# Kernel tuning notes

Measured on AMD Instinct MI355X. Metric: run time of the kernel, lower is better.

The kernel has to match this reference:

```python
import jax, jax.numpy as jnp
import numpy as np

N_NODES = 50000


def _gcn_layer(x, src, dst, norm_src, norm_dst, W, b, act):
    # DGL GraphConv with norm='both': D_out^{-1/2} A D_in^{-1/2} X W + b
    h = x * norm_src[:, None]                      # scale by src out-degree
    m = h[src]                                     # gather messages [E, d]
    agg = jax.ops.segment_sum(m, dst, num_segments=N_NODES)  # scatter-add
    agg = agg * norm_dst[:, None]
    out = agg @ W + b
    if act:
        out = jax.nn.relu(out)
    return out


def setup_inputs() -> dict:
    key = jax.random.key(0)
    ks = jax.random.split(key, 10)
    E = 800000
    in_size, hid, out_size = 128, 128, 64
    features = jax.random.normal(ks[0], (N_NODES, in_size), dtype=jnp.float32)
    src = jax.random.randint(ks[1], (E,), 0, N_NODES, dtype=jnp.int32)
    dst = jax.random.randint(ks[2], (E,), 0, N_NODES, dtype=jnp.int32)
    s = 0.05
    W1 = jax.random.normal(ks[3], (in_size, hid), dtype=jnp.float32) * s
    b1 = jnp.zeros((hid,), dtype=jnp.float32)
    W2 = jax.random.normal(ks[4], (hid, hid), dtype=jnp.float32) * s
    b2 = jnp.zeros((hid,), dtype=jnp.float32)
    W3 = jax.random.normal(ks[5], (hid, out_size), dtype=jnp.float32) * s
    b3 = jnp.zeros((out_size,), dtype=jnp.float32)
    return {"features": features, "W1": W1, "b1": b1, "W2": W2, "b2": b2,
            "W3": W3, "b3": b3, "src": src, "dst": dst}


def reference(features, W1, b1, W2, b2, W3, b3, src, dst):
    ones = jnp.ones(src.shape, dtype=features.dtype)
    out_deg = jax.ops.segment_sum(ones, src, num_segments=N_NODES)
    in_deg = jax.ops.segment_sum(ones, dst, num_segments=N_NODES)
    norm_src = jnp.maximum(out_deg, 1.0) ** -0.5   # clamp(min=1) as in DGL
    norm_dst = jnp.maximum(in_deg, 1.0) ** -0.5
    h = _gcn_layer(features, src, dst, norm_src, norm_dst, W1, b1, act=True)
    # dropout is identity in eval mode
    h = _gcn_layer(h, src, dst, norm_src, norm_dst, W2, b2, act=True)
    h = _gcn_layer(h, src, dst, norm_src, norm_dst, W3, b3, act=False)
    return h
```

## Files before the change

kernel.cpp:

```cpp
#include <hip/hip_runtime.h>
#include <math.h>

#define N_NODES 50000
#define K_DIM 128
#define CAP 64
#define CHUNK 12500
#define RH 25000
#define HWORDS 12500

typedef __attribute__((ext_vector_type(8))) short short8_t;
typedef __attribute__((ext_vector_type(8))) unsigned short ushort8_t;
typedef __attribute__((ext_vector_type(4))) float f32x4_t;
typedef __attribute__((ext_vector_type(8))) _Float16 half8_t;

__device__ inline unsigned short f2bf(float x) {
    unsigned u = __float_as_uint(x);
    unsigned r = u + 0x7fffu + ((u >> 16) & 1u);
    return (unsigned short)(r >> 16);
}
__device__ inline float bf2f(unsigned short h) {
    return __uint_as_float(((unsigned)h) << 16);
}

__global__ __launch_bounds__(1024) void hist_init_split_kernel(
        const int* __restrict__ src, const int* __restrict__ dst, int E,
        unsigned* __restrict__ pin, unsigned* __restrict__ pout,
        _Float16* Yx, _Float16* Yy, _Float16* Yz,
        const float* __restrict__ W1, const float* __restrict__ W2,
        const float* __restrict__ W3,
        unsigned short* __restrict__ W1h, unsigned short* __restrict__ W1l,
        unsigned short* __restrict__ W2h, unsigned short* __restrict__ W2l,
        unsigned short* __restrict__ W3h, unsigned short* __restrict__ W3l,
        int NBLK) {
    int tid = threadIdx.x;
    if (blockIdx.x < (unsigned)(NBLK * 4)) {
        __shared__ unsigned h[HWORDS];
        int b  = blockIdx.x >> 2;
        int io = (blockIdx.x >> 1) & 1;
        int r  = blockIdx.x & 1;
        for (int t = tid; t < HWORDS; t += 1024) h[t] = 0;
        __syncthreads();
        const int* keys = io ? src : dst;
        int start = b * CHUNK;
        int end = start + CHUNK; if (end > E) end = E;
        int vlo = r * RH;
        for (int i = start + tid; i < end; i += 1024) {
            int v = keys[i] - vlo;
            if ((unsigned)v < (unsigned)RH)
                atomicAdd(&h[v >> 1], 1u << ((v & 1) * 16));
        }
        __syncthreads();
        unsigned* out = io ? pout : pin;
        for (int t = tid; t < HWORDS; t += 1024)
            out[(size_t)b * (2 * HWORDS) + r * HWORDS + t] = h[t];
        return;
    }
    if (blockIdx.x == (unsigned)(NBLK * 4)) {
        if (tid < 128) {
            Yx[(size_t)N_NODES * 128 + tid] = (_Float16)0.f;
            Yy[(size_t)N_NODES * 128 + tid] = (_Float16)0.f;
        }
        if (tid < 64) Yz[(size_t)N_NODES * 64 + tid] = (_Float16)0.f;
        return;
    }
    int gi = (blockIdx.x - (NBLK * 4 + 1)) * 1024 + tid;
    const float* W; unsigned short *WBh, *WBl; int M, i;
    if (gi < 2048)      { W = W1; WBh = W1h; WBl = W1l; M = 128; i = gi; }
    else if (gi < 4096) { W = W2; WBh = W2h; WBl = W2l; M = 128; i = gi - 2048; }
    else if (gi < 5120) { W = W3; WBh = W3h; WBl = W3l; M = 64;  i = gi - 4096; }
    else return;
    int c    = i >> 8;
    int rem  = i & 255;
    int kc   = rem >> 6;
    int lane = rem & 63;
    int m = lane & 15, q = lane >> 4;
    int n = c * 16 + m;
    #pragma unroll
    for (int j = 0; j < 8; ++j) {
        int k = kc * 32 + q * 8 + j;
        float w = W[(size_t)k * M + n];
        unsigned short hi = f2bf(w);
        unsigned short lo = f2bf(w - bf2f(hi));
        WBh[(size_t)i * 8 + j] = hi;
        WBl[(size_t)i * 8 + j] = lo;
    }
}

__global__ void offsets_norm_kernel(const unsigned* __restrict__ pin,
                                    const unsigned* __restrict__ pout,
                                    unsigned short* __restrict__ off16,
                                    int* __restrict__ indeg,
                                    float* __restrict__ nsrc, float* __restrict__ ndst,
                                    int n, int NB) {
    int v = blockIdx.x * blockDim.x + threadIdx.x;
    if (v >= n) return;
    int wi = v >> 1, sh = (v & 1) * 16;
    int od = 0;
    for (int b = 0; b < NB; ++b)
        od += (pout[(size_t)b * (2 * HWORDS) + wi] >> sh) & 0xffff;
    int run = 0;
    for (int b = 0; b < NB; ++b) {
        int c = (pin[(size_t)b * (2 * HWORDS) + wi] >> sh) & 0xffff;
        off16[(size_t)b * n + v] = (unsigned short)(run < CAP ? run : CAP);
        run += c;
    }
    indeg[v] = run < CAP ? run : CAP;
    int odc = od < 1 ? 1 : od;
    int idc = run < 1 ? 1 : run;
    nsrc[v] = 1.0f / sqrtf((float)odc);
    ndst[v] = 1.0f / sqrtf((float)idc);
}

__global__ __launch_bounds__(512) void scatter_gemm_kernel(
        const int* __restrict__ src, const int* __restrict__ dst, int E,
        const unsigned short* __restrict__ off16,
        unsigned short* __restrict__ csr, int n, int NB2,
        const float* __restrict__ X,
        const unsigned short* __restrict__ WBh_,
        const unsigned short* __restrict__ WBl_,
        const float* __restrict__ nsrc, _Float16* __restrict__ Yh) {
    __shared__ unsigned smemu[17408];
    int tid = threadIdx.x;

    if (blockIdx.x < (unsigned)NB2) {
        unsigned* cur = smemu;
        int b = blockIdx.x >> 1;
        int r = blockIdx.x & 1;
        int vlo = r * RH;
        const unsigned short* offb = off16 + (size_t)b * n + vlo;
        for (int t = tid; t < HWORDS; t += 512)
            cur[t] = (unsigned)offb[2 * t] | ((unsigned)offb[2 * t + 1] << 16);
        __syncthreads();
        int start = b * CHUNK;
        int end = start + CHUNK; if (end > E) end = E;
        for (int i = start + tid; i < end; i += 512) {
            int v = dst[i];
            int vr = v - vlo;
            if ((unsigned)vr < (unsigned)RH) {
                int sh = (vr & 1) * 16;
                unsigned old = atomicAdd(&cur[vr >> 1], 1u << sh);
                unsigned p = (old >> sh) & 0xffff;
                if (p < CAP) csr[((size_t)v << 6) + p] = (unsigned short)src[i];
            }
        }
        return;
    }

    constexpr int LSTR = 136;
    int s    = tid >> 8;
    int stid = tid & 255;
    short* Xhi = (short*)smemu + s * 17408;
    short* Xlo = Xhi + 64 * LSTR;
    int gb = blockIdx.x - NB2;
    int rowBlock = gb * 128 + s * 64;
    int lane = stid & 63, wave = stid >> 6;

    #pragma unroll
    for (int l = 0; l < 8; ++l) {
        int idx = (stid + l * 256) * 4;
        int r = idx >> 7;
        int c = idx & 127;
        float4 v = make_float4(0.f, 0.f, 0.f, 0.f);
        int gr = rowBlock + r;
        if (gr < n) v = *(const float4*)&X[(size_t)gr * K_DIM + c];
        unsigned short h0 = f2bf(v.x), h1 = f2bf(v.y), h2 = f2bf(v.z), h3 = f2bf(v.w);
        short4 hs = {(short)h0, (short)h1, (short)h2, (short)h3};
        short4 ls = {(short)f2bf(v.x - bf2f(h0)), (short)f2bf(v.y - bf2f(h1)),
                     (short)f2bf(v.z - bf2f(h2)), (short)f2bf(v.w - bf2f(h3))};
        *(short4*)&Xhi[r * LSTR + c] = hs;
        *(short4*)&Xlo[r * LSTR + c] = ls;
    }
    __syncthreads();

    int m = lane & 15, q = lane >> 4;
    short8_t ah[4], al[4];
    {
        int abase = (wave * 16 + m) * LSTR + q * 8;
        #pragma unroll
        for (int kc = 0; kc < 4; ++kc) {
            ah[kc] = *(const short8_t*)&Xhi[abase + kc * 32];
            al[kc] = *(const short8_t*)&Xlo[abase + kc * 32];
        }
    }
    float ns[4];
    int orow0 = rowBlock + wave * 16 + q * 4;
    #pragma unroll
    for (int r = 0; r < 4; ++r) ns[r] = (orow0 + r < n) ? nsrc[orow0 + r] : 0.f;

    const short8_t* WBh = (const short8_t*)WBh_;
    const short8_t* WBl = (const short8_t*)WBl_;
    #pragma unroll
    for (int c = 0; c < 8; ++c) {
        short8_t bh[4], bl[4];
        #pragma unroll
        for (int kc = 0; kc < 4; ++kc) {
            bh[kc] = WBh[(c * 4 + kc) * 64 + lane];
            bl[kc] = WBl[(c * 4 + kc) * 64 + lane];
        }
        f32x4_t acc = {0.f, 0.f, 0.f, 0.f};
        #pragma unroll
        for (int kc = 0; kc < 4; ++kc) {
            acc = __builtin_amdgcn_mfma_f32_16x16x32_bf16(ah[kc], bh[kc], acc, 0, 0, 0);
            acc = __builtin_amdgcn_mfma_f32_16x16x32_bf16(ah[kc], bl[kc], acc, 0, 0, 0);
            acc = __builtin_amdgcn_mfma_f32_16x16x32_bf16(al[kc], bh[kc], acc, 0, 0, 0);
        }
        int col = c * 16 + m;
        #pragma unroll
        for (int r = 0; r < 4; ++r) {
            int row = orow0 + r;
            if (row < n) Yh[(size_t)row * 128 + col] = (_Float16)(acc[r] * ns[r]);
        }
    }
}

template <int MOUT>
__global__ __launch_bounds__(256, 3) void agg_gemm_kernel(
        const _Float16* __restrict__ Yin,
        const int* __restrict__ indeg, const unsigned short* __restrict__ csr,
        const float* __restrict__ ndst, const float* __restrict__ bias,
        const unsigned short* __restrict__ WBh_,
        const unsigned short* __restrict__ WBl_,
        const float* __restrict__ nsrc, _Float16* __restrict__ Yout, int n) {
    constexpr int LSTR = 136;
    __shared__ short Xhi[32 * LSTR];
    __shared__ short Xlo[32 * LSTR];
    int tid = threadIdx.x;
    int lane = tid & 63, wave = tid >> 6;
    int rowBlock = blockIdx.x * 32;

    int sub = tid >> 4;
    int f8  = (tid & 15) * 8;
    #pragma unroll 1
    for (int p = 0; p < 2; ++p) {
        int r = p * 16 + sub;
        int v = rowBlock + r;
        float o[8] = {};
        if (v < n) {
            int deg = indeg[v];
            const unsigned short* __restrict__ row = &csr[(size_t)v * CAP];
            float acc[8] = {};
            #pragma unroll 1
            for (int i = 0; i < deg; i += 16) {
                ushort8_t ia = *(const ushort8_t*)&row[i];
                ushort8_t ib = *(const ushort8_t*)&row[i + 8];
                int idx[16];
                #pragma unroll
                for (int t = 0; t < 8; ++t) idx[t] = (int)ia[t];
                #pragma unroll
                for (int t = 0; t < 8; ++t) idx[8 + t] = (int)ib[t];
                #pragma unroll
                for (int t = 1; t < 16; ++t)
                    if (i + t >= deg) idx[t] = N_NODES;
                half8_t g[16];
                #pragma unroll
                for (int t = 0; t < 16; ++t)
                    g[t] = *(const half8_t*)&Yin[(size_t)idx[t] * 128 + f8];
                #pragma unroll
                for (int t = 0; t < 16; ++t) {
                    #pragma unroll
                    for (int j = 0; j < 8; ++j) acc[j] += (float)g[t][j];
                }
            }
            float nd = ndst[v];
            #pragma unroll
            for (int j = 0; j < 8; ++j)
                o[j] = fmaxf(nd * acc[j] + bias[f8 + j], 0.f);
        }
        short hs[8], ls[8];
        #pragma unroll
        for (int j = 0; j < 8; ++j) {
            unsigned short h = f2bf(o[j]);
            hs[j] = (short)h;
            ls[j] = (short)f2bf(o[j] - bf2f(h));
        }
        *(short4*)&Xhi[r * LSTR + f8]     = *(short4*)&hs[0];
        *(short4*)&Xhi[r * LSTR + f8 + 4] = *(short4*)&hs[4];
        *(short4*)&Xlo[r * LSTR + f8]     = *(short4*)&ls[0];
        *(short4*)&Xlo[r * LSTR + f8 + 4] = *(short4*)&ls[4];
    }
    __syncthreads();

    int m = lane & 15, q = lane >> 4;
    int wrow = wave & 1;
    int wcol = wave >> 1;
    short8_t ah[4], al[4];
    {
        int abase = (wrow * 16 + m) * LSTR + q * 8;
        #pragma unroll
        for (int kc = 0; kc < 4; ++kc) {
            ah[kc] = *(const short8_t*)&Xhi[abase + kc * 32];
            al[kc] = *(const short8_t*)&Xlo[abase + kc * 32];
        }
    }
    float ns[4];
    int orow0 = rowBlock + wrow * 16 + q * 4;
    #pragma unroll
    for (int r = 0; r < 4; ++r) ns[r] = (orow0 + r < n) ? nsrc[orow0 + r] : 0.f;

    const short8_t* WBh = (const short8_t*)WBh_;
    const short8_t* WBl = (const short8_t*)WBl_;
    constexpr int CTH = MOUT / 32;
    #pragma unroll
    for (int c2 = 0; c2 < CTH; ++c2) {
        int c = wcol * CTH + c2;
        short8_t bh[4], bl[4];
        #pragma unroll
        for (int kc = 0; kc < 4; ++kc) {
            bh[kc] = WBh[(c * 4 + kc) * 64 + lane];
            bl[kc] = WBl[(c * 4 + kc) * 64 + lane];
        }
        f32x4_t acc = {0.f, 0.f, 0.f, 0.f};
        #pragma unroll
        for (int kc = 0; kc < 4; ++kc) {
            acc = __builtin_amdgcn_mfma_f32_16x16x32_bf16(ah[kc], bh[kc], acc, 0, 0, 0);
            acc = __builtin_amdgcn_mfma_f32_16x16x32_bf16(ah[kc], bl[kc], acc, 0, 0, 0);
            acc = __builtin_amdgcn_mfma_f32_16x16x32_bf16(al[kc], bh[kc], acc, 0, 0, 0);
        }
        int col = c * 16 + m;
        #pragma unroll
        for (int r = 0; r < 4; ++r) {
            int row = orow0 + r;
            if (row < n) Yout[(size_t)row * MOUT + col] = (_Float16)(acc[r] * ns[r]);
        }
    }
}

template <int M, bool RELU>
__global__ __launch_bounds__(256, 3) void agg_kernel(const _Float16* __restrict__ Y,
                                                     const int* __restrict__ indeg,
                                                     const unsigned short* __restrict__ csr,
                                                     const float* __restrict__ ndst,
                                                     const float* __restrict__ bias,
                                                     float* __restrict__ Z, int n) {
    constexpr int LPN = M / 8;
    constexpr int NPB = 256 / LPN;
    int v = blockIdx.x * NPB + threadIdx.x / LPN;
    if (v >= n) return;
    int f8 = (threadIdx.x % LPN) * 8;
    int deg = indeg[v];
    const unsigned short* __restrict__ row = &csr[(size_t)v * CAP];
    float acc[8] = {};
    #pragma unroll 1
    for (int i = 0; i < deg; i += 16) {
        ushort8_t ia = *(const ushort8_t*)&row[i];
        ushort8_t ib = *(const ushort8_t*)&row[i + 8];
        int idx[16];
        #pragma unroll
        for (int t = 0; t < 8; ++t) idx[t] = (int)ia[t];
        #pragma unroll
        for (int t = 0; t < 8; ++t) idx[8 + t] = (int)ib[t];
        #pragma unroll
        for (int t = 1; t < 16; ++t)
            if (i + t >= deg) idx[t] = N_NODES;
        half8_t g[16];
        #pragma unroll
        for (int t = 0; t < 16; ++t)
            g[t] = *(const half8_t*)&Y[(size_t)idx[t] * M + f8];
        #pragma unroll
        for (int t = 0; t < 16; ++t) {
            #pragma unroll
            for (int j = 0; j < 8; ++j) acc[j] += (float)g[t][j];
        }
    }
    float nd = ndst[v];
    float4 bb0 = *(const float4*)&bias[f8];
    float4 bb1 = *(const float4*)&bias[f8 + 4];
    float o[8];
    o[0] = nd * acc[0] + bb0.x; o[1] = nd * acc[1] + bb0.y;
    o[2] = nd * acc[2] + bb0.z; o[3] = nd * acc[3] + bb0.w;
    o[4] = nd * acc[4] + bb1.x; o[5] = nd * acc[5] + bb1.y;
    o[6] = nd * acc[6] + bb1.z; o[7] = nd * acc[7] + bb1.w;
    if (RELU) {
        #pragma unroll
        for (int j = 0; j < 8; ++j) o[j] = fmaxf(o[j], 0.f);
    }
    *(float4*)&Z[(size_t)v * M + f8]     = make_float4(o[0], o[1], o[2], o[3]);
    *(float4*)&Z[(size_t)v * M + f8 + 4] = make_float4(o[4], o[5], o[6], o[7]);
}


extern "C" void kernel_launch(void* const* d_in, const int* in_sizes, int n_in,
                              void* d_out, int out_size, void* d_ws, size_t ws_size,
                              hipStream_t stream) {
    const float* features = (const float*)d_in[0];
    const float* W1 = (const float*)d_in[1];
    const float* b1 = (const float*)d_in[2];
    const float* W2 = (const float*)d_in[3];
    const float* b2 = (const float*)d_in[4];
    const float* W3 = (const float*)d_in[5];
    const float* b3 = (const float*)d_in[6];
    const int* src = (const int*)d_in[7];
    const int* dst = (const int*)d_in[8];
    const int E = in_sizes[7];
    const int N = N_NODES;
    const int NB = (E + CHUNK - 1) / CHUNK;

    char* w = (char*)d_ws;
    auto alloc = [&](size_t bytes) {
        char* p = w;
        w += (bytes + 255) & ~(size_t)255;
        return p;
    };
    _Float16* Yx = (_Float16*)alloc((size_t)(N + 1) * 128 * 2);
    _Float16* Yy = (_Float16*)alloc((size_t)(N + 1) * 128 * 2);
    _Float16* Yz = (_Float16*)alloc((size_t)(N + 1) * 64 * 2);
    unsigned short* csr = (unsigned short*)alloc((size_t)N * CAP * 2);
    unsigned* pin  = (unsigned*)alloc((size_t)NB * 2 * HWORDS * 4);
    unsigned* pout = (unsigned*)alloc((size_t)NB * 2 * HWORDS * 4);
    unsigned short* off16 = (unsigned short*)alloc((size_t)NB * N * 2);
    int*   indeg  = (int*)alloc((size_t)N * 4);
    float* nsrc   = (float*)alloc((size_t)N * 4);
    float* ndst   = (float*)alloc((size_t)N * 4);
    unsigned short* W1h = (unsigned short*)alloc(128 * 128 * 2);
    unsigned short* W1l = (unsigned short*)alloc(128 * 128 * 2);
    unsigned short* W2h = (unsigned short*)alloc(128 * 128 * 2);
    unsigned short* W2l = (unsigned short*)alloc(128 * 128 * 2);
    unsigned short* W3h = (unsigned short*)alloc(64 * 128 * 2);
    unsigned short* W3l = (unsigned short*)alloc(64 * 128 * 2);

    hist_init_split_kernel<<<NB * 4 + 1 + 5, 1024, 0, stream>>>(
        src, dst, E, pin, pout, Yx, Yy, Yz,
        W1, W2, W3, W1h, W1l, W2h, W2l, W3h, W3l, NB);
    offsets_norm_kernel<<<(N + 255) / 256, 256, 0, stream>>>(pin, pout, off16, indeg,
                                                             nsrc, ndst, N, NB);
    int gemmBlocks = (N + 127) / 128;
    scatter_gemm_kernel<<<NB * 2 + gemmBlocks, 512, 0, stream>>>(
        src, dst, E, off16, csr, N, NB * 2,
        features, W1h, W1l, nsrc, Yx);

    int gblocks32 = (N + 31) / 32;
    agg_gemm_kernel<128><<<gblocks32, 256, 0, stream>>>(Yx, indeg, csr, ndst, b1,
                                                        W2h, W2l, nsrc, Yy, N);
    agg_gemm_kernel<64><<<gblocks32, 256, 0, stream>>>(Yy, indeg, csr, ndst, b2,
                                                       W3h, W3l, nsrc, Yz, N);
    agg_kernel<64, false><<<gblocks32, 256, 0, stream>>>(Yz, indeg, csr, ndst, b3,
                                                         (float*)d_out, N);
}
```

Measured before the change: 228.7 us.

## Overlap first-layer GEMM with degree histogram and apply source norm during gather

The first X·W1 GEMM no longer depends on the source-degree norm, so it moves out of the scatter kernel and shares one launch with the histogram blocks, which now run at 256 threads. The nsrc scaling moves into the first aggregation, where each gathered neighbour row is scaled by its nsrc value. The weight split moves into a small separate prep kernel, and a padding entry nsrc[N] = 0 is added for the dummy index. The aim is to shorten the critical path by running the GEMM alongside the histogram, at the cost of an extra per-edge nsrc load and FMA in layer 1 and one more kernel launch.

```diff
diff --git a/kernel.cpp b/kernel.cpp
--- a/kernel.cpp
+++ b/kernel.cpp
@@ -22,48 +22,24 @@
     return __uint_as_float(((unsigned)h) << 16);
 }
 
-__global__ __launch_bounds__(1024) void hist_init_split_kernel(
-        const int* __restrict__ src, const int* __restrict__ dst, int E,
-        unsigned* __restrict__ pin, unsigned* __restrict__ pout,
-        _Float16* Yx, _Float16* Yy, _Float16* Yz,
+__global__ __launch_bounds__(256) void prep_w_kernel(
         const float* __restrict__ W1, const float* __restrict__ W2,
         const float* __restrict__ W3,
         unsigned short* __restrict__ W1h, unsigned short* __restrict__ W1l,
         unsigned short* __restrict__ W2h, unsigned short* __restrict__ W2l,
         unsigned short* __restrict__ W3h, unsigned short* __restrict__ W3l,
-        int NBLK) {
-    int tid = threadIdx.x;
-    if (blockIdx.x < (unsigned)(NBLK * 4)) {
-        __shared__ unsigned h[HWORDS];
-        int b  = blockIdx.x >> 2;
-        int io = (blockIdx.x >> 1) & 1;
-        int r  = blockIdx.x & 1;
-        for (int t = tid; t < HWORDS; t += 1024) h[t] = 0;
-        __syncthreads();
-        const int* keys = io ? src : dst;
-        int start = b * CHUNK;
-        int end = start + CHUNK; if (end > E) end = E;
-        int vlo = r * RH;
-        for (int i = start + tid; i < end; i += 1024) {
-            int v = keys[i] - vlo;
-            if ((unsigned)v < (unsigned)RH)
-                atomicAdd(&h[v >> 1], 1u << ((v & 1) * 16));
-        }
-        __syncthreads();
-        unsigned* out = io ? pout : pin;
-        for (int t = tid; t < HWORDS; t += 1024)
-            out[(size_t)b * (2 * HWORDS) + r * HWORDS + t] = h[t];
-        return;
-    }
-    if (blockIdx.x == (unsigned)(NBLK * 4)) {
+        _Float16* Yx, _Float16* Yy, _Float16* Yz, float* __restrict__ nsrc) {
+    int b = blockIdx.x, tid = threadIdx.x;
+    if (b == 20) {
         if (tid < 128) {
             Yx[(size_t)N_NODES * 128 + tid] = (_Float16)0.f;
             Yy[(size_t)N_NODES * 128 + tid] = (_Float16)0.f;
         }
         if (tid < 64) Yz[(size_t)N_NODES * 64 + tid] = (_Float16)0.f;
+        if (tid == 200) nsrc[N_NODES] = 0.f;
         return;
     }
-    int gi = (blockIdx.x - (NBLK * 4 + 1)) * 1024 + tid;
+    int gi = b * 256 + tid;
     const float* W; unsigned short *WBh, *WBl; int M, i;
     if (gi < 2048)      { W = W1; WBh = W1h; WBl = W1l; M = 128; i = gi; }
     else if (gi < 4096) { W = W2; WBh = W2h; WBl = W2l; M = 128; i = gi - 2048; }
@@ -86,6 +62,100 @@
     }
 }
 
+__global__ __launch_bounds__(256) void hist_gemm_kernel(
+        const int* __restrict__ src, const int* __restrict__ dst, int E,
+        unsigned* __restrict__ pin, unsigned* __restrict__ pout,
+        int NBLK,
+        const float* __restrict__ X,
+        const unsigned short* __restrict__ WBh_,
+        const unsigned short* __restrict__ WBl_,
+        _Float16* __restrict__ Yh, int n) {
+    __shared__ __attribute__((aligned(16))) unsigned smem[HWORDS];
+    int tid = threadIdx.x;
+
+    if (blockIdx.x < (unsigned)(NBLK * 4)) {
+        int b  = blockIdx.x >> 2;
+        int io = (blockIdx.x >> 1) & 1;
+        int r  = blockIdx.x & 1;
+        for (int t = tid; t < HWORDS; t += 256) smem[t] = 0;
+        __syncthreads();
+        const int* keys = io ? src : dst;
+        int start = b * CHUNK;
+        int end = start + CHUNK; if (end > E) end = E;
+        int vlo = r * RH;
+        for (int i = start + tid; i < end; i += 256) {
+            int v = keys[i] - vlo;
+            if ((unsigned)v < (unsigned)RH)
+                atomicAdd(&smem[v >> 1], 1u << ((v & 1) * 16));
+        }
+        __syncthreads();
+        unsigned* out = io ? pout : pin;
+        for (int t = tid; t < HWORDS; t += 256)
+            out[(size_t)b * (2 * HWORDS) + r * HWORDS + t] = smem[t];
+        return;
+    }
+
+    constexpr int LSTR = 136;
+    short* Xhi = (short*)smem;
+    short* Xlo = Xhi + 64 * LSTR;
+    int lane = tid & 63, wave = tid >> 6;
+    int rowBlock = (blockIdx.x - NBLK * 4) * 64;
+
+    #pragma unroll
+    for (int l = 0; l < 8; ++l) {
+        int idx = (tid + l * 256) * 4;
+        int r = idx >> 7;
+        int c = idx & 127;
+        float4 v = make_float4(0.f, 0.f, 0.f, 0.f);
+        int gr = rowBlock + r;
+        if (gr < n) v = *(const float4*)&X[(size_t)gr * K_DIM + c];
+        unsigned short h0 = f2bf(v.x), h1 = f2bf(v.y), h2 = f2bf(v.z), h3 = f2bf(v.w);
+        short4 hs = {(short)h0, (short)h1, (short)h2, (short)h3};
+        short4 ls = {(short)f2bf(v.x - bf2f(h0)), (short)f2bf(v.y - bf2f(h1)),
+                     (short)f2bf(v.z - bf2f(h2)), (short)f2bf(v.w - bf2f(h3))};
+        *(short4*)&Xhi[r * LSTR + c] = hs;
+        *(short4*)&Xlo[r * LSTR + c] = ls;
+    }
+    __syncthreads();
+
+    int m = lane & 15, q = lane >> 4;
+    short8_t ah[4], al[4];
+    {
+        int abase = (wave * 16 + m) * LSTR + q * 8;
+        #pragma unroll
+        for (int kc = 0; kc < 4; ++kc) {
+            ah[kc] = *(const short8_t*)&Xhi[abase + kc * 32];
+            al[kc] = *(const short8_t*)&Xlo[abase + kc * 32];
+        }
+    }
+    int orow0 = rowBlock + wave * 16 + q * 4;
+
+    const short8_t* WBh = (const short8_t*)WBh_;
+    const short8_t* WBl = (const short8_t*)WBl_;
+    #pragma unroll
+    for (int c = 0; c < 8; ++c) {
+        short8_t bh[4], bl[4];
+        #pragma unroll
+        for (int kc = 0; kc < 4; ++kc) {
+            bh[kc] = WBh[(c * 4 + kc) * 64 + lane];
+            bl[kc] = WBl[(c * 4 + kc) * 64 + lane];
+        }
+        f32x4_t acc = {0.f, 0.f, 0.f, 0.f};
+        #pragma unroll
+        for (int kc = 0; kc < 4; ++kc) {
+            acc = __builtin_amdgcn_mfma_f32_16x16x32_bf16(ah[kc], bh[kc], acc, 0, 0, 0);
+            acc = __builtin_amdgcn_mfma_f32_16x16x32_bf16(ah[kc], bl[kc], acc, 0, 0, 0);
+            acc = __builtin_amdgcn_mfma_f32_16x16x32_bf16(al[kc], bh[kc], acc, 0, 0, 0);
+        }
+        int col = c * 16 + m;
+        #pragma unroll
+        for (int r = 0; r < 4; ++r) {
+            int row = orow0 + r;
+            if (row < n) Yh[(size_t)row * 128 + col] = (_Float16)acc[r];
+        }
+    }
+}
+
 __global__ void offsets_norm_kernel(const unsigned* __restrict__ pin,
                                     const unsigned* __restrict__ pout,
                                     unsigned short* __restrict__ off16,
@@ -111,116 +181,42 @@
     ndst[v] = 1.0f / sqrtf((float)idc);
 }
 
-__global__ __launch_bounds__(512) void scatter_gemm_kernel(
+__global__ __launch_bounds__(512) void scatter_kernel(
         const int* __restrict__ src, const int* __restrict__ dst, int E,
         const unsigned short* __restrict__ off16,
-        unsigned short* __restrict__ csr, int n, int NB2,
-        const float* __restrict__ X,
-        const unsigned short* __restrict__ WBh_,
-        const unsigned short* __restrict__ WBl_,
-        const float* __restrict__ nsrc, _Float16* __restrict__ Yh) {
-    __shared__ unsigned smemu[17408];
+        unsigned short* __restrict__ csr, int n) {
+    __shared__ unsigned cur[HWORDS];
     int tid = threadIdx.x;
-
-    if (blockIdx.x < (unsigned)NB2) {
-        unsigned* cur = smemu;
-        int b = blockIdx.x >> 1;
-        int r = blockIdx.x & 1;
-        int vlo = r * RH;
-        const unsigned short* offb = off16 + (size_t)b * n + vlo;
-        for (int t = tid; t < HWORDS; t += 512)
-            cur[t] = (unsigned)offb[2 * t] | ((unsigned)offb[2 * t + 1] << 16);
-        __syncthreads();
-        int start = b * CHUNK;
-        int end = start + CHUNK; if (end > E) end = E;
-        for (int i = start + tid; i < end; i += 512) {
-            int v = dst[i];
-            int vr = v - vlo;
-            if ((unsigned)vr < (unsigned)RH) {
-                int sh = (vr & 1) * 16;
-                unsigned old = atomicAdd(&cur[vr >> 1], 1u << sh);
-                unsigned p = (old >> sh) & 0xffff;
-                if (p < CAP) csr[((size_t)v << 6) + p] = (unsigned short)src[i];
-            }
-        }
-        return;
-    }
-
-    constexpr int LSTR = 136;
-    int s    = tid >> 8;
-    int stid = tid & 255;
-    short* Xhi = (short*)smemu + s * 17408;
-    short* Xlo = Xhi + 64 * LSTR;
-    int gb = blockIdx.x - NB2;
-    int rowBlock = gb * 128 + s * 64;
-    int lane = stid & 63, wave = stid >> 6;
-
-    #pragma unroll
-    for (int l = 0; l < 8; ++l) {
-        int idx = (stid + l * 256) * 4;
-        int r = idx >> 7;
-        int c = idx & 127;
-        float4 v = make_float4(0.f, 0.f, 0.f, 0.f);
-        int gr = rowBlock + r;
-        if (gr < n) v = *(const float4*)&X[(size_t)gr * K_DIM + c];
-        unsigned short h0 = f2bf(v.x), h1 = f2bf(v.y), h2 = f2bf(v.z), h3 = f2bf(v.w);
-        short4 hs = {(short)h0, (short)h1, (short)h2, (short)h3};
-        short4 ls = {(short)f2bf(v.x - bf2f(h0)), (short)f2bf(v.y - bf2f(h1)),
-                     (short)f2bf(v.z - bf2f(h2)), (short)f2bf(v.w - bf2f(h3))};
-        *(short4*)&Xhi[r * LSTR + c] = hs;
-        *(short4*)&Xlo[r * LSTR + c] = ls;
-    }
+    int b = blockIdx.x >> 1;
+    int r = blockIdx.x & 1;
+    int vlo = r * RH;
+    const unsigned short* offb = off16 + (size_t)b * n + vlo;
+    for (int t = tid; t < HWORDS; t += 512)
+        cur[t] = (unsigned)offb[2 * t] | ((unsigned)offb[2 * t + 1] << 16);
     __syncthreads();
-
-    int m = lane & 15, q = lane >> 4;
-    short8_t ah[4], al[4];
-    {
-        int abase = (wave * 16 + m) * LSTR + q * 8;
-        #pragma unroll
-        for (int kc = 0; kc < 4; ++kc) {
-            ah[kc] = *(const short8_t*)&Xhi[abase + kc * 32];
-            al[kc] = *(const short8_t*)&Xlo[abase + kc * 32];
-        }
-    }
-    float ns[4];
-    int orow0 = rowBlock + wave * 16 + q * 4;
-    #pragma unroll
-    for (int r = 0; r < 4; ++r) ns[r] = (orow0 + r < n) ? nsrc[orow0 + r] : 0.f;
-
-    const short8_t* WBh = (const short8_t*)WBh_;
-    const short8_t* WBl = (const short8_t*)WBl_;
-    #pragma unroll
-    for (int c = 0; c < 8; ++c) {
-        short8_t bh[4], bl[4];
-        #pragma unroll
-        for (int kc = 0; kc < 4; ++kc) {
-            bh[kc] = WBh[(c * 4 + kc) * 64 + lane];
-            bl[kc] = WBl[(c * 4 + kc) * 64 + lane];
-        }
-        f32x4_t acc = {0.f, 0.f, 0.f, 0.f};
-        #pragma unroll
-        for (int kc = 0; kc < 4; ++kc) {
-            acc = __builtin_amdgcn_mfma_f32_16x16x32_bf16(ah[kc], bh[kc], acc, 0, 0, 0);
-            acc = __builtin_amdgcn_mfma_f32_16x16x32_bf16(ah[kc], bl[kc], acc, 0, 0, 0);
-            acc = __builtin_amdgcn_mfma_f32_16x16x32_bf16(al[kc], bh[kc], acc, 0, 0, 0);
-        }
-        int col = c * 16 + m;
-        #pragma unroll
-        for (int r = 0; r < 4; ++r) {
-            int row = orow0 + r;
-            if (row < n) Yh[(size_t)row * 128 + col] = (_Float16)(acc[r] * ns[r]);
-        }
-    }
-}
-
-template <int MOUT>
+    int start = b * CHUNK;
+    int end = start + CHUNK; if (end > E) end = E;
+    for (int i = start + tid; i < end; i += 512) {
+        int v = dst[i];
+        int vr = v - vlo;
+        if ((unsigned)vr < (unsigned)RH) {
+            int sh = (vr & 1) * 16;
+            unsigned old = atomicAdd(&cur[vr >> 1], 1u << sh);
+            unsigned p = (old >> sh) & 0xffff;
+            if (p < CAP) csr[((size_t)v << 6) + p] = (unsigned short)src[i];
+        }
+    }
+}
+
+template <int MOUT, bool NSG>
 __global__ __launch_bounds__(256, 3) void agg_gemm_kernel(
         const _Float16* __restrict__ Yin,
         const int* __restrict__ indeg, const unsigned short* __restrict__ csr,
         const float* __restrict__ ndst, const float* __restrict__ bias,
         const unsigned short* __restrict__ WBh_,
         const unsigned short* __restrict__ WBl_,
-        const float* __restrict__ nsrc, _Float16* __restrict__ Yout, int n) {
+        const float* __restrict__ nsrc,
+        _Float16* __restrict__ Yout, int n) {
     constexpr int LSTR = 136;
     __shared__ short Xhi[32 * LSTR];
     __shared__ short Xlo[32 * LSTR];
@@ -251,14 +247,24 @@
                 #pragma unroll
                 for (int t = 1; t < 16; ++t)
                     if (i + t >= deg) idx[t] = N_NODES;
+                float ns_[16];
+                if (NSG) {
+                    #pragma unroll
+                    for (int t = 0; t < 16; ++t) ns_[t] = nsrc[idx[t]];
+                }
                 half8_t g[16];
                 #pragma unroll
                 for (int t = 0; t < 16; ++t)
                     g[t] = *(const half8_t*)&Yin[(size_t)idx[t] * 128 + f8];
                 #pragma unroll
                 for (int t = 0; t < 16; ++t) {
-                    #pragma unroll
-                    for (int j = 0; j < 8; ++j) acc[j] += (float)g[t][j];
+                    if (NSG) {
+                        #pragma unroll
+                        for (int j = 0; j < 8; ++j) acc[j] = fmaf(ns_[t], (float)g[t][j], acc[j]);
+                    } else {
+                        #pragma unroll
+                        for (int j = 0; j < 8; ++j) acc[j] += (float)g[t][j];
+                    }
                 }
             }
             float nd = ndst[v];
@@ -409,7 +415,7 @@
     unsigned* pout = (unsigned*)alloc((size_t)NB * 2 * HWORDS * 4);
     unsigned short* off16 = (unsigned short*)alloc((size_t)NB * N * 2);
     int*   indeg  = (int*)alloc((size_t)N * 4);
-    float* nsrc   = (float*)alloc((size_t)N * 4);
+    float* nsrc   = (float*)alloc((size_t)(N + 1) * 4);
     float* ndst   = (float*)alloc((size_t)N * 4);
     unsigned short* W1h = (unsigned short*)alloc(128 * 128 * 2);
     unsigned short* W1l = (unsigned short*)alloc(128 * 128 * 2);
@@ -418,21 +424,20 @@
     unsigned short* W3h = (unsigned short*)alloc(64 * 128 * 2);
     unsigned short* W3l = (unsigned short*)alloc(64 * 128 * 2);
 
-    hist_init_split_kernel<<<NB * 4 + 1 + 5, 1024, 0, stream>>>(
-        src, dst, E, pin, pout, Yx, Yy, Yz,
-        W1, W2, W3, W1h, W1l, W2h, W2l, W3h, W3l, NB);
+    int gb64 = (N + 63) / 64;
+    int gblocks32 = (N + 31) / 32;
+
+    prep_w_kernel<<<21, 256, 0, stream>>>(W1, W2, W3, W1h, W1l, W2h, W2l, W3h, W3l,
+                                          Yx, Yy, Yz, nsrc);
+    hist_gemm_kernel<<<NB * 4 + gb64, 256, 0, stream>>>(
+        src, dst, E, pin, pout, NB, features, W1h, W1l, Yx, N);
     offsets_norm_kernel<<<(N + 255) / 256, 256, 0, stream>>>(pin, pout, off16, indeg,
                                                              nsrc, ndst, N, NB);
-    int gemmBlocks = (N + 127) / 128;
-    scatter_gemm_kernel<<<NB * 2 + gemmBlocks, 512, 0, stream>>>(
-        src, dst, E, off16, csr, N, NB * 2,
-        features, W1h, W1l, nsrc, Yx);
-
-    int gblocks32 = (N + 31) / 32;
-    agg_gemm_kernel<128><<<gblocks32, 256, 0, stream>>>(Yx, indeg, csr, ndst, b1,
-                                                        W2h, W2l, nsrc, Yy, N);
-    agg_gemm_kernel<64><<<gblocks32, 256, 0, stream>>>(Yy, indeg, csr, ndst, b2,
-                                                       W3h, W3l, nsrc, Yz, N);
+    scatter_kernel<<<NB * 2, 512, 0, stream>>>(src, dst, E, off16, csr, N);
+    agg_gemm_kernel<128, true><<<gblocks32, 256, 0, stream>>>(Yx, indeg, csr, ndst, b1,
+                                                              W2h, W2l, nsrc, Yy, N);
+    agg_gemm_kernel<64, false><<<gblocks32, 256, 0, stream>>>(Yy, indeg, csr, ndst, b2,
+                                                              W3h, W3l, nsrc, Yz, N);
     agg_kernel<64, false><<<gblocks32, 256, 0, stream>>>(Yz, indeg, csr, ndst, b3,
                                                          (float*)d_out, N);
 }
```

After: 248.3 us. 1.09x slower.
